# Kernel tuning notes

Measured on AMD Instinct MI355X. Metric: run time of the kernel, lower is better.

## Reference

```python
import jax, jax.numpy as jnp
import numpy as np

E = 512
H = 8
DH = E // H
LN_EPS = 1e-5


def setup_inputs() -> dict:
    key = jax.random.key(0)
    ks = jax.random.split(key, 8)
    s = 1.0 / np.sqrt(E)
    return {
        "query": jax.random.normal(ks[0], (2, 2048, E), jnp.float32),
        "key_value": jax.random.normal(ks[1], (2, 4096, E), jnp.float32),
        "Wq": jax.random.normal(ks[2], (E, E), jnp.float32) * s,
        "bq": jnp.zeros((E,), jnp.float32),
        "Wk": jax.random.normal(ks[3], (E, E), jnp.float32) * s,
        "bk": jnp.zeros((E,), jnp.float32),
        "Wv": jax.random.normal(ks[4], (E, E), jnp.float32) * s,
        "bv": jnp.zeros((E,), jnp.float32),
        "Wo": jax.random.normal(ks[5], (E, E), jnp.float32) * s,
        "bo": jnp.zeros((E,), jnp.float32),
        "ln_gamma": jnp.ones((E,), jnp.float32),
        "ln_beta": jnp.zeros((E,), jnp.float32),
    }


def reference(query, key_value, Wq, bq, Wk, bk, Wv, bv, Wo, bo, ln_gamma, ln_beta):
    B, Lq, _ = query.shape
    Lk = key_value.shape[1]
    # Projections (torch Linear: x @ W.T + b)
    q = (query @ Wq.T + bq).reshape(B, Lq, H, DH)
    k = (key_value @ Wk.T + bk).reshape(B, Lk, H, DH)
    v = (key_value @ Wv.T + bv).reshape(B, Lk, H, DH)
    scale = 1.0 / np.sqrt(DH).astype(np.float32)
    scores = jnp.einsum("bqhd,bkhd->bhqk", q, k) * scale  # [B,H,Lq,Lk]
    attn = jax.nn.softmax(scores, axis=-1)
    ctx = jnp.einsum("bhqk,bkhd->bqhd", attn, v).reshape(B, Lq, E)
    attn_out = ctx @ Wo.T + bo
    # residual + LayerNorm (dropout is identity in eval)
    x = query + attn_out
    mu = jnp.mean(x, axis=-1, keepdims=True)
    var = jnp.mean(jnp.square(x - mu), axis=-1, keepdims=True)
    return (x - mu) * jax.lax.rsqrt(var + LN_EPS) * ln_gamma + ln_beta
```

## Files before the change

kernel.cpp:

```cpp
#include <hip/hip_runtime.h>
#include <hip/hip_bf16.h>

typedef __bf16 bf16;
typedef __bf16 bf16x8 __attribute__((ext_vector_type(8)));
typedef __bf16 bf16x4 __attribute__((ext_vector_type(4)));
typedef float f32x4 __attribute__((ext_vector_type(4)));

#define MFMA16(a, b, c) __builtin_amdgcn_mfma_f32_16x16x32_bf16((a), (b), (c), 0, 0, 0)

constexpr int LQ = 2048, LK = 4096, E = 512, H = 8, DH = 64;
#define QSCALE 0.1803368801111137f

#if __has_builtin(__builtin_amdgcn_exp2f)
#define EXP2(x) __builtin_amdgcn_exp2f(x)
#else
#define EXP2(x) __expf(0.6931471805599453f * (x))
#endif

__device__ __forceinline__ bf16x8 ld8(const bf16* p) { return *(const bf16x8*)p; }

__global__ __launch_bounds__(256) void cvt4_kernel(
    const float* __restrict__ w0, const float* __restrict__ w1,
    const float* __restrict__ w2, const float* __restrict__ w3,
    bf16* __restrict__ dst) {
  const float* srcs[4] = {w0, w1, w2, w3};
  const float* src = srcs[blockIdx.y];
  bf16* d = dst + (size_t)blockIdx.y * 262144;
  int i = (blockIdx.x * 256 + threadIdx.x) * 4;
  f32x4 v = *(const f32x4*)(src + i);
  bf16x4 o;
  for (int j = 0; j < 4; ++j) o[j] = (bf16)v[j];
  *(bf16x4*)(d + i) = o;
}

__global__ __launch_bounds__(256) void proj_gemm_kernel(
    const float* __restrict__ query, const float* __restrict__ kv,
    const bf16* __restrict__ Wall,
    const float* __restrict__ bq, const float* __restrict__ bk,
    const float* __restrict__ bv,
    bf16* __restrict__ qproj, bf16* __restrict__ kproj, bf16* __restrict__ vt) {
  __shared__ bf16 smA[2][128][72];
  __shared__ bf16 smB[2][128][72];
  const int tid = threadIdx.x;
  const int lane = tid & 63, wave = tid >> 6;
  const int lrow = lane & 15, quad = lane >> 4;
  const int wm = wave & 1, wn = wave >> 1;

  int x = blockIdx.x, z, mt;
  if (x < 32) { z = 0; mt = x; }
  else if (x < 96) { z = 1; mt = x - 32; }
  else { z = 2; mt = x - 96; }
  const float* A = ((z == 0) ? query : kv) + (size_t)mt * 128 * E;
  const bf16* W = Wall + (size_t)z * 262144;
  const float* bias = (z == 0) ? bq : (z == 1) ? bk : bv;
  const int n0 = blockIdx.y * 128;

  const int arow = tid >> 4, acol = tid & 15;
  const int brow = tid >> 3, bcol = tid & 7;

  f32x4 pa[8];
  bf16x8 pb[4];
#define LOAD_T(t)                                                             \
  {                                                                           \
    for (int p = 0; p < 8; ++p)                                               \
      pa[p] = *(const f32x4*)(A + (size_t)(p * 16 + arow) * E + (t) * 64 +    \
                              acol * 4);                                      \
    for (int p = 0; p < 4; ++p)                                               \
      pb[p] = ld8(W + (size_t)(n0 + p * 32 + brow) * E + (t) * 64 + bcol * 8);\
  }
#define STORE_T(bs)                                                           \
  {                                                                           \
    for (int p = 0; p < 8; ++p) {                                             \
      bf16x4 av;                                                              \
      for (int e = 0; e < 4; ++e) av[e] = (bf16)pa[p][e];                     \
      *(bf16x4*)&smA[bs][p * 16 + arow][acol * 4] = av;                       \
    }                                                                         \
    for (int p = 0; p < 4; ++p)                                               \
      *(bf16x8*)&smB[bs][p * 32 + brow][bcol * 8] = pb[p];                    \
  }

  LOAD_T(0);
  STORE_T(0);
  LOAD_T(1);
  __syncthreads();

  f32x4 acc[4][4] = {};
  for (int t = 0; t < 8; ++t) {
    const int bs = t & 1;
    bf16x8 af[2][4], bfr[2][4];
    for (int ks = 0; ks < 2; ++ks)
      for (int i = 0; i < 4; ++i)
        af[ks][i] = ld8(&smA[bs][wm * 64 + 16 * i + lrow][ks * 32 + quad * 8]);
    for (int ks = 0; ks < 2; ++ks)
      for (int c = 0; c < 4; ++c)
        bfr[ks][c] = ld8(&smB[bs][wn * 64 + 16 * c + lrow][ks * 32 + quad * 8]);
    for (int ks = 0; ks < 2; ++ks)
      for (int i = 0; i < 4; ++i)
        for (int c = 0; c < 4; ++c)
          acc[i][c] = MFMA16(af[ks][i], bfr[ks][c], acc[i][c]);
    if (t < 7) {
      STORE_T(bs ^ 1);
      if (t < 6) LOAD_T(t + 2);
    }
    __syncthreads();
  }
#undef LOAD_T
#undef STORE_T

  const float qsc = (z == 0) ? QSCALE : 1.f;
  float bvl[4];
  for (int c = 0; c < 4; ++c) bvl[c] = bias[n0 + wn * 64 + 16 * c + lrow];
  bf16* Cs = &smA[0][0][0];
  for (int i = 0; i < 4; ++i)
    for (int c = 0; c < 4; ++c)
      for (int r = 0; r < 4; ++r) {
        int row = wm * 64 + 16 * i + 4 * quad + r;
        int col = wn * 64 + 16 * c + lrow;
        bf16 val = (bf16)((acc[i][c][r] + bvl[c]) * qsc);
        if (z < 2) Cs[row * 136 + col] = val;
        else       Cs[col * 136 + row] = val;
      }
  __syncthreads();
  const int rr = tid >> 1, hh = tid & 1;
  if (z < 2) {
    bf16* Y = (z == 0) ? qproj : kproj;
    bf16* dstp = Y + (size_t)(mt * 128 + rr) * E + n0 + hh * 64;
    for (int j = 0; j < 8; ++j)
      *(bf16x8*)(dstp + j * 8) = *(bf16x8*)&Cs[rr * 136 + hh * 64 + j * 8];
  } else {
    int m0g = mt * 128, b = m0g >> 12, kk0 = m0g & 4095;
    int ng = n0 + rr, hd = ng >> 6, d = ng & 63;
    bf16* dstp = vt + ((size_t)((b * 8 + hd) * 64 + d)) * LK + kk0 + hh * 64;
    for (int j = 0; j < 8; ++j)
      *(bf16x8*)(dstp + j * 8) = *(bf16x8*)&Cs[rr * 136 + hh * 64 + j * 8];
  }
}

__global__ __launch_bounds__(256, 2) void attn_kernel(
    const bf16* __restrict__ qp, const bf16* __restrict__ kp,
    const bf16* __restrict__ vtg, bf16* __restrict__ ctx) {
  const int tid = threadIdx.x;
  const int lane = tid & 63, wave = tid >> 6;
  const int lrow = lane & 15, quad = lane >> 4;
  const int hw = blockIdx.x;
  const int xcd = hw & 7, ii = hw >> 3;
  const int bh = xcd * 2 + (ii >> 5), qt = ii & 31;
  const int b = bh >> 3, h = bh & 7;
  const int q0 = qt * 64;

  __shared__ __align__(16) char smem[70656];
  bf16* Ks = (bf16*)(smem + wave * 13568);
  bf16* Vs = Ks + 2048;
  bf16* Ps = Vs + 2048;

  bf16x8 qf[4][2];
  for (int g = 0; g < 4; ++g)
    for (int s = 0; s < 2; ++s)
      qf[g][s] = ld8(qp + (size_t)(b * LQ + q0 + 16 * g + lrow) * E + h * DH +
                     32 * s + quad * 8);

  float lrun[4] = {0.f, 0.f, 0.f, 0.f};
  f32x4 acc[4][4] = {};

  const int kkbase = wave * 1024;
  const int krow_ = lane >> 3, kg_ = lane & 7;
  const int vrow_ = lane >> 2, vg_ = lane & 3;
  const bf16* kgp =
      kp + ((size_t)b * LK + kkbase + krow_) * E + h * DH + kg_ * 8;
  const bf16* vgp = vtg + ((size_t)bh * DH + vrow_) * LK + kkbase + vg_ * 8;
  const int kws = (kg_ ^ krow_) * 8;
  const int vws = (vg_ ^ ((vrow_ >> 1) & 3)) * 8;

  bf16x8 pk[4], pv[4];
#define GLOAD(it)                                                   \
  for (int j = 0; j < 4; ++j) {                                     \
    pk[j] = ld8(kgp + ((size_t)(it)*32 + j * 8) * E);               \
    pv[j] = ld8(vgp + (size_t)j * 16 * LK + (it)*32);               \
  }
#define STAGE()                                                     \
  for (int j = 0; j < 4; ++j) {                                     \
    *(bf16x8*)&Ks[(j * 8 + krow_) * 64 + kws] = pk[j];              \
    *(bf16x8*)&Vs[(j * 16 + vrow_) * 32 + vws] = pv[j];             \
  }

  GLOAD(0);
  STAGE();
  for (int it = 0; it < 32; ++it) {
    if (it < 31) GLOAD(it + 1);

    bf16x8 kf[2][2], vf[4];
    for (int kt = 0; kt < 2; ++kt)
      for (int sd = 0; sd < 2; ++sd)
        kf[kt][sd] = ld8(
            &Ks[(16 * kt + lrow) * 64 + ((sd * 4 + quad) ^ (lrow & 7)) * 8]);
    for (int c = 0; c < 4; ++c)
      vf[c] =
          ld8(&Vs[(16 * c + lrow) * 32 + (quad ^ ((lrow >> 1) & 3)) * 8]);

    f32x4 st[4][2];
    __builtin_amdgcn_s_setprio(1);
    for (int g = 0; g < 4; ++g)
      for (int kt = 0; kt < 2; ++kt) {
        st[g][kt] = (f32x4){0.f, 0.f, 0.f, 0.f};
        st[g][kt] = MFMA16(kf[kt][0], qf[g][0], st[g][kt]);
        st[g][kt] = MFMA16(kf[kt][1], qf[g][1], st[g][kt]);
      }
    __builtin_amdgcn_s_setprio(0);
    for (int g = 0; g < 4; ++g)
      for (int kt = 0; kt < 2; ++kt) {
        bf16x4 pp;
        for (int r = 0; r < 4; ++r) {
          float p = EXP2(st[g][kt][r]);
          lrun[g] += p;
          pp[r] = (bf16)p;
        }
        *(bf16x4*)&Ps[(16 * g + lrow) * 40 + 16 * kt + 4 * quad] = pp;
      }
    __builtin_amdgcn_s_setprio(1);
    for (int g = 0; g < 4; ++g) {
      bf16x8 pf = ld8(&Ps[(16 * g + lrow) * 40 + quad * 8]);
      for (int c = 0; c < 4; ++c) acc[g][c] = MFMA16(pf, vf[c], acc[g][c]);
    }
    __builtin_amdgcn_s_setprio(0);
    if (it < 31) STAGE();
  }
#undef GLOAD
#undef STAGE

  for (int g = 0; g < 4; ++g) {
    lrun[g] += __shfl_xor(lrun[g], 16);
    lrun[g] += __shfl_xor(lrun[g], 32);
  }
  __syncthreads();
  float* F = (float*)smem;
  float* Lr = (float*)(smem + 69632);
  for (int g = 0; g < 4; ++g)
    for (int c = 0; c < 4; ++c)
      for (int r = 0; r < 4; ++r)
        F[(wave * 64 + 16 * g + 4 * quad + r) * 68 + 16 * c + lrow] =
            acc[g][c][r];
  if (lane < 16)
    for (int g = 0; g < 4; ++g) Lr[wave * 64 + 16 * g + lrow] = lrun[g];
  __syncthreads();
  {
    const int q = tid >> 2, d0 = (tid & 3) * 16;
    float ls = Lr[q] + Lr[64 + q] + Lr[128 + q] + Lr[192 + q];
    float inv = 1.f / ls;
    float o[16] = {};
    for (int w = 0; w < 4; ++w) {
      const float* Fr = &F[(w * 64 + q) * 68 + d0];
      for (int j = 0; j < 16; j += 4) {
        f32x4 x = *(const f32x4*)(Fr + j);
        o[j] += x[0];
        o[j + 1] += x[1];
        o[j + 2] += x[2];
        o[j + 3] += x[3];
      }
    }
    bf16* dst = ctx + (size_t)(b * LQ + q0 + q) * E + h * DH + d0;
    bf16x8 ov0, ov1;
    for (int j = 0; j < 8; ++j) {
      ov0[j] = (bf16)(o[j] * inv);
      ov1[j] = (bf16)(o[8 + j] * inv);
    }
    *(bf16x8*)dst = ov0;
    *(bf16x8*)(dst + 8) = ov1;
  }
}

__global__ __launch_bounds__(512) void outln_kernel(
    const bf16* __restrict__ Cx, const bf16* __restrict__ Wo,
    const float* __restrict__ bo, const float* __restrict__ resid,
    const float* __restrict__ gamma, const float* __restrict__ beta,
    float* __restrict__ out) {
  const int tid = threadIdx.x;
  const int lane = tid & 63, wave = tid >> 6;
  const int lrow = lane & 15, quad = lane >> 4;
  const int m0 = blockIdx.x * 16;
  const int n0 = wave * 64;

  __shared__ bf16 As[16][520];
  __shared__ bf16 Wos[512][72];
  __shared__ float red1[16][8], red2[16][8];
  {
    int r = tid >> 5, ch = tid & 31;
    const bf16* src = Cx + (size_t)(m0 + r) * E + ch * 16;
    *(bf16x8*)&As[r][ch * 16] = ld8(src);
    *(bf16x8*)&As[r][ch * 16 + 8] = ld8(src + 8);
  }
  const int wr = tid >> 3, wc = tid & 7;
  bf16x8 pw[8];
  for (int p = 0; p < 8; ++p)
    pw[p] = ld8(Wo + (size_t)(p * 64 + wr) * E + wc * 8);
  __syncthreads();

  f32x4 acc[4] = {};
  for (int t = 0; t < 8; ++t) {
    for (int p = 0; p < 8; ++p)
      *(bf16x8*)&Wos[p * 64 + wr][wc * 8] = pw[p];
    __syncthreads();
    if (t < 7)
      for (int p = 0; p < 8; ++p)
        pw[p] = ld8(Wo + (size_t)(p * 64 + wr) * E + (t + 1) * 64 + wc * 8);
    for (int ks = 0; ks < 2; ++ks) {
      bf16x8 a = *(const bf16x8*)&As[lrow][t * 64 + ks * 32 + quad * 8];
      for (int c = 0; c < 4; ++c) {
        bf16x8 w = *(const bf16x8*)&Wos[n0 + 16 * c + lrow][ks * 32 + quad * 8];
        acc[c] = MFMA16(a, w, acc[c]);
      }
    }
    __syncthreads();
  }

  float s1[4] = {}, s2[4] = {};
  for (int c = 0; c < 4; ++c) {
    int n = n0 + 16 * c + lrow;
    float bb = bo[n];
    for (int r = 0; r < 4; ++r) {
      int m = 4 * quad + r;
      float xv = acc[c][r] + bb + resid[(size_t)(m0 + m) * E + n];
      acc[c][r] = xv;
      s1[r] += xv;
      s2[r] += xv * xv;
    }
  }
  for (int off = 1; off < 16; off <<= 1)
    for (int r = 0; r < 4; ++r) {
      s1[r] += __shfl_xor(s1[r], off);
      s2[r] += __shfl_xor(s2[r], off);
    }
  if (lrow == 0)
    for (int r = 0; r < 4; ++r) {
      red1[4 * quad + r][wave] = s1[r];
      red2[4 * quad + r][wave] = s2[r];
    }
  __syncthreads();
  float mu[4], rstd[4];
  for (int r = 0; r < 4; ++r) {
    int m = 4 * quad + r;
    float t1 = 0.f, t2 = 0.f;
    for (int w = 0; w < 8; ++w) { t1 += red1[m][w]; t2 += red2[m][w]; }
    float mean = t1 * (1.f / 512.f);
    float var = t2 * (1.f / 512.f) - mean * mean;
    mu[r] = mean;
    rstd[r] = rsqrtf(var + 1e-5f);
  }
  for (int c = 0; c < 4; ++c) {
    int n = n0 + 16 * c + lrow;
    float gm = gamma[n], bt = beta[n];
    for (int r = 0; r < 4; ++r) {
      int m = m0 + 4 * quad + r;
      out[(size_t)m * E + n] = (acc[c][r] - mu[r]) * rstd[r] * gm + bt;
    }
  }
}

extern "C" void kernel_launch(void* const* d_in, const int* in_sizes, int n_in,
                              void* d_out, int out_size, void* d_ws, size_t ws_size,
                              hipStream_t stream) {
  const float* query     = (const float*)d_in[0];
  const float* key_value = (const float*)d_in[1];
  const float* Wq = (const float*)d_in[2];
  const float* bq = (const float*)d_in[3];
  const float* Wk = (const float*)d_in[4];
  const float* bk = (const float*)d_in[5];
  const float* Wv = (const float*)d_in[6];
  const float* bv = (const float*)d_in[7];
  const float* Wo = (const float*)d_in[8];
  const float* bo = (const float*)d_in[9];
  const float* gamma = (const float*)d_in[10];
  const float* beta  = (const float*)d_in[11];
  float* out = (float*)d_out;

  bf16* Wb    = (bf16*)d_ws;
  bf16* Wob   = Wb + (size_t)3 * 262144;
  bf16* qproj = Wb + (size_t)4 * 262144;
  bf16* kproj = qproj + (size_t)4096 * 512;
  bf16* vt    = kproj + (size_t)8192 * 512;

  cvt4_kernel<<<dim3(256, 4), 256, 0, stream>>>(Wq, Wk, Wv, Wo, Wb);
  proj_gemm_kernel<<<dim3(160, 4), 256, 0, stream>>>(
      query, key_value, Wb, bq, bk, bv, qproj, kproj, vt);
  attn_kernel<<<512, 256, 0, stream>>>(qproj, kproj, vt, qproj );
  outln_kernel<<<256, 512, 0, stream>>>(qproj, Wob, bo, query, gamma, beta, out);
}
```

Baseline: 178.3 us.

## Switch attention to 32x32 MFMA with in-register P via permlane32 swap

Moves the attention inner loop from 16x16x32 to 32x32x16 bf16 MFMA tiles. The softmax probabilities are packed with v_cvt_pk_bf16_f32 and rearranged across lane halves with v_permlane32_swap, so P no longer goes through LDS. This removes the per-iteration Ps shared-memory write and read, shrinks per-wave LDS, and changes the V swizzle to match the new fragment layout. The risks are higher register pressure from the 16-wide accumulators and reliance on gfx950-specific inline asm.

```diff
diff --git a/kernel.cpp b/kernel.cpp
--- a/kernel.cpp
+++ b/kernel.cpp
@@ -5,8 +5,11 @@
 typedef __bf16 bf16x8 __attribute__((ext_vector_type(8)));
 typedef __bf16 bf16x4 __attribute__((ext_vector_type(4)));
 typedef float f32x4 __attribute__((ext_vector_type(4)));
+typedef float f32x16 __attribute__((ext_vector_type(16)));
+typedef unsigned int u32x4 __attribute__((ext_vector_type(4)));
 
 #define MFMA16(a, b, c) __builtin_amdgcn_mfma_f32_16x16x32_bf16((a), (b), (c), 0, 0, 0)
+#define MFMA32(a, b, c) __builtin_amdgcn_mfma_f32_32x32x16_bf16((a), (b), (c), 0, 0, 0)
 
 constexpr int LQ = 2048, LK = 4096, E = 512, H = 8, DH = 64;
 #define QSCALE 0.1803368801111137f
@@ -141,7 +144,7 @@
     const bf16* __restrict__ vtg, bf16* __restrict__ ctx) {
   const int tid = threadIdx.x;
   const int lane = tid & 63, wave = tid >> 6;
-  const int lrow = lane & 15, quad = lane >> 4;
+  const int l31 = lane & 31, hi = lane >> 5;
   const int hw = blockIdx.x;
   const int xcd = hw & 7, ii = hw >> 3;
   const int bh = xcd * 2 + (ii >> 5), qt = ii & 31;
@@ -149,18 +152,17 @@
   const int q0 = qt * 64;
 
   __shared__ __align__(16) char smem[70656];
-  bf16* Ks = (bf16*)(smem + wave * 13568);
+  bf16* Ks = (bf16*)(smem + wave * 8192);
   bf16* Vs = Ks + 2048;
-  bf16* Ps = Vs + 2048;
-
-  bf16x8 qf[4][2];
-  for (int g = 0; g < 4; ++g)
-    for (int s = 0; s < 2; ++s)
-      qf[g][s] = ld8(qp + (size_t)(b * LQ + q0 + 16 * g + lrow) * E + h * DH +
-                     32 * s + quad * 8);
-
-  float lrun[4] = {0.f, 0.f, 0.f, 0.f};
-  f32x4 acc[4][4] = {};
+
+  bf16x8 qf[2][4];
+  for (int t = 0; t < 2; ++t)
+    for (int st = 0; st < 4; ++st)
+      qf[t][st] = ld8(qp + (size_t)(b * LQ + q0 + 32 * t + l31) * E + h * DH +
+                      st * 16 + hi * 8);
+
+  float lp[2] = {0.f, 0.f};
+  f32x16 acc[2][2] = {};
 
   const int kkbase = wave * 1024;
   const int krow_ = lane >> 3, kg_ = lane & 7;
@@ -169,7 +171,7 @@
       kp + ((size_t)b * LK + kkbase + krow_) * E + h * DH + kg_ * 8;
   const bf16* vgp = vtg + ((size_t)bh * DH + vrow_) * LK + kkbase + vg_ * 8;
   const int kws = (kg_ ^ krow_) * 8;
-  const int vws = (vg_ ^ ((vrow_ >> 1) & 3)) * 8;
+  const int vws = (vg_ ^ (vrow_ & 3)) * 8;
 
   bf16x8 pk[4], pv[4];
 #define GLOAD(it)                                                   \
@@ -188,67 +190,86 @@
   for (int it = 0; it < 32; ++it) {
     if (it < 31) GLOAD(it + 1);
 
-    bf16x8 kf[2][2], vf[4];
-    for (int kt = 0; kt < 2; ++kt)
-      for (int sd = 0; sd < 2; ++sd)
-        kf[kt][sd] = ld8(
-            &Ks[(16 * kt + lrow) * 64 + ((sd * 4 + quad) ^ (lrow & 7)) * 8]);
-    for (int c = 0; c < 4; ++c)
-      vf[c] =
-          ld8(&Vs[(16 * c + lrow) * 32 + (quad ^ ((lrow >> 1) & 3)) * 8]);
-
-    f32x4 st[4][2];
-    __builtin_amdgcn_s_setprio(1);
-    for (int g = 0; g < 4; ++g)
-      for (int kt = 0; kt < 2; ++kt) {
-        st[g][kt] = (f32x4){0.f, 0.f, 0.f, 0.f};
-        st[g][kt] = MFMA16(kf[kt][0], qf[g][0], st[g][kt]);
-        st[g][kt] = MFMA16(kf[kt][1], qf[g][1], st[g][kt]);
+    bf16x8 kf[4], vf[2][2];
+#pragma unroll
+    for (int st = 0; st < 4; ++st)
+      kf[st] = ld8(&Ks[l31 * 64 + ((st * 2 + hi) ^ (l31 & 7)) * 8]);
+#pragma unroll
+    for (int dt = 0; dt < 2; ++dt)
+      for (int s = 0; s < 2; ++s)
+        vf[dt][s] =
+            ld8(&Vs[(dt * 32 + l31) * 32 + ((s * 2 + hi) ^ (l31 & 3)) * 8]);
+
+#pragma unroll
+    for (int t = 0; t < 2; ++t) {
+      f32x16 s_ = {};
+      __builtin_amdgcn_s_setprio(1);
+      s_ = MFMA32(kf[0], qf[t][0], s_);
+      s_ = MFMA32(kf[1], qf[t][1], s_);
+      s_ = MFMA32(kf[2], qf[t][2], s_);
+      s_ = MFMA32(kf[3], qf[t][3], s_);
+      __builtin_amdgcn_s_setprio(0);
+      unsigned w[4][2];
+#pragma unroll
+      for (int t4 = 0; t4 < 4; ++t4)
+#pragma unroll
+        for (int u = 0; u < 2; ++u) {
+          float e0 = EXP2(s_[4 * t4 + 2 * u]);
+          float e1 = EXP2(s_[4 * t4 + 2 * u + 1]);
+          lp[t] += e0;
+          lp[t] += e1;
+          asm("v_cvt_pk_bf16_f32 %0, %1, %2"
+              : "=v"(w[t4][u])
+              : "v"(e0), "v"(e1));
+        }
+      bf16x8 paf[2];
+#pragma unroll
+      for (int s = 0; s < 2; ++s) {
+        unsigned a0 = w[2 * s][0], b0 = w[2 * s + 1][0];
+        unsigned a1 = w[2 * s][1], b1 = w[2 * s + 1][1];
+        asm("v_permlane32_swap_b32 %0, %1" : "+v"(a0), "+v"(b0));
+        asm("v_permlane32_swap_b32 %0, %1" : "+v"(a1), "+v"(b1));
+        u32x4 pw_ = {a0, a1, b0, b1};
+        paf[s] = *(bf16x8*)&pw_;
       }
-    __builtin_amdgcn_s_setprio(0);
-    for (int g = 0; g < 4; ++g)
-      for (int kt = 0; kt < 2; ++kt) {
-        bf16x4 pp;
-        for (int r = 0; r < 4; ++r) {
-          float p = EXP2(st[g][kt][r]);
-          lrun[g] += p;
-          pp[r] = (bf16)p;
-        }
-        *(bf16x4*)&Ps[(16 * g + lrow) * 40 + 16 * kt + 4 * quad] = pp;
-      }
-    __builtin_amdgcn_s_setprio(1);
-    for (int g = 0; g < 4; ++g) {
-      bf16x8 pf = ld8(&Ps[(16 * g + lrow) * 40 + quad * 8]);
-      for (int c = 0; c < 4; ++c) acc[g][c] = MFMA16(pf, vf[c], acc[g][c]);
-    }
-    __builtin_amdgcn_s_setprio(0);
-    if (it < 31) STAGE();
+      __builtin_amdgcn_s_setprio(1);
+#pragma unroll
+      for (int dt = 0; dt < 2; ++dt)
+        for (int s = 0; s < 2; ++s)
+          acc[t][dt] = MFMA32(paf[s], vf[dt][s], acc[t][dt]);
+      __builtin_amdgcn_s_setprio(0);
+
+      if (t == 0 && it < 31) STAGE();
+    }
   }
 #undef GLOAD
 #undef STAGE
 
-  for (int g = 0; g < 4; ++g) {
-    lrun[g] += __shfl_xor(lrun[g], 16);
-    lrun[g] += __shfl_xor(lrun[g], 32);
-  }
+  for (int t = 0; t < 2; ++t) lp[t] += __shfl_xor(lp[t], 32);
+
   __syncthreads();
   float* F = (float*)smem;
   float* Lr = (float*)(smem + 69632);
-  for (int g = 0; g < 4; ++g)
-    for (int c = 0; c < 4; ++c)
-      for (int r = 0; r < 4; ++r)
-        F[(wave * 64 + 16 * g + 4 * quad + r) * 68 + 16 * c + lrow] =
-            acc[g][c][r];
-  if (lane < 16)
-    for (int g = 0; g < 4; ++g) Lr[wave * 64 + 16 * g + lrow] = lrun[g];
+#pragma unroll
+  for (int t = 0; t < 2; ++t)
+    for (int dt = 0; dt < 2; ++dt)
+#pragma unroll
+      for (int r = 0; r < 16; ++r) {
+        int q = 32 * t + (r & 3) + 8 * (r >> 2) + 4 * hi;
+        F[(wave * 64 + q) * 68 + dt * 32 + l31] = acc[t][dt][r];
+      }
+  if (hi == 0) {
+    Lr[wave * 64 + l31] = lp[0];
+    Lr[wave * 64 + 32 + l31] = lp[1];
+  }
   __syncthreads();
   {
     const int q = tid >> 2, d0 = (tid & 3) * 16;
     float ls = Lr[q] + Lr[64 + q] + Lr[128 + q] + Lr[192 + q];
     float inv = 1.f / ls;
     float o[16] = {};
-    for (int w = 0; w < 4; ++w) {
-      const float* Fr = &F[(w * 64 + q) * 68 + d0];
+    for (int w2 = 0; w2 < 4; ++w2) {
+      const float* Fr = &F[(w2 * 64 + q) * 68 + d0];
       for (int j = 0; j < 16; j += 4) {
         f32x4 x = *(const f32x4*)(Fr + j);
         o[j] += x[0];
```

Result: no change. 176.2 us (-1.1%).
